# Kernel tuning notes

Hardware: AMD Instinct MI355X
Metric: run time of the kernel (lower is better)

The kernel has to match this reference:

```python
import jax, jax.numpy as jnp
import numpy as np

N_BLADES = 8

def _build_cayley():
    """Geometric-product table for Cl(3,0): C[i,j,k] s.t. (e_i * e_j) = sum_k C[i,j,k] e_k.
    Blade order: [1, e1, e2, e3, e12, e13, e23, e123] via bitmasks [0,1,2,4,3,5,6,7]."""
    blades = [0, 1, 2, 4, 3, 5, 6, 7]
    idx = {b: i for i, b in enumerate(blades)}
    C = np.zeros((8, 8, 8), dtype=np.float32)
    for i, a in enumerate(blades):
        for j, b in enumerate(blades):
            aa = a >> 1
            cnt = 0
            while aa:
                cnt += bin(aa & b).count('1')
                aa >>= 1
            sign = -1.0 if (cnt & 1) else 1.0
            C[i, j, idx[a ^ b]] += sign
    return jnp.asarray(C)

CAYLEY = _build_cayley()

def clifford_linear(x, w, b):
    # x: (..., 8), w: (8,), b: (8,) -> geometric product w * x + b
    return jnp.einsum('ijk,i,...j->...k', CAYLEY, w, x) + b

def setup_inputs() -> dict:
    key = jax.random.key(0)
    ks = jax.random.split(key, 9)
    B, S = 4, 4096
    inp = {'x': jax.random.normal(ks[0], (B, S, N_BLADES), dtype=jnp.float32)}
    names = ['wq', 'bq', 'wk', 'bk', 'wv', 'bv', 'wo', 'bo']
    for i, n in enumerate(names):
        scale = 1.0 / np.sqrt(N_BLADES) if n.startswith('w') else 0.02
        inp[n] = jax.random.normal(ks[i + 1], (N_BLADES,), dtype=jnp.float32) * scale
    return inp

def reference(x, wq, bq, wk, bk, wv, bv, wo, bo):
    # head_dim = max(1, 8 // 2) = 4 -> scale = sqrt(4) = 2
    scale = jnp.float32(2.0)
    Q = clifford_linear(x, wq, bq)  # (B,S,8)
    K = clifford_linear(x, wk, bk)
    V = clifford_linear(x, wv, bv)
    c0 = CAYLEY[..., 0]  # (8,8) scalar part of geometric product
    attn = jnp.einsum('ij,bsi,btj->bst', c0, Q, K) / scale  # (B,S,S)
    attn = jax.nn.softmax(attn, axis=-1)
    out = jnp.einsum('bst,btk->bsk', attn, V)  # (B,S,8)
    return clifford_linear(out, wo, bo)
```

## Files before the change

kernel.cpp:

```cpp
#include <hip/hip_runtime.h>
#include <math.h>

#define SEQ 4096
#define NBATCH 4
#define SGRP 64
#define TWAVES 16
#define TCHUNK (SEQ / TWAVES)
#define TT 32
#define VTILE 288

typedef _Float16 f16;
typedef __attribute__((ext_vector_type(8))) _Float16 f16x8;
typedef __attribute__((ext_vector_type(8))) __bf16 bf16x8;
typedef __attribute__((ext_vector_type(16))) float f32x16;
typedef __attribute__((ext_vector_type(4))) unsigned u32x4;
typedef __attribute__((ext_vector_type(2))) unsigned u32x2;

__device__ __forceinline__ float fexp2(float x) {
#if __has_builtin(__builtin_amdgcn_exp2f)
  return __builtin_amdgcn_exp2f(x);
#else
  return exp2f(x);
#endif
}

__device__ __forceinline__ u32x2 pswap(unsigned a, unsigned b) {
#if __has_builtin(__builtin_amdgcn_permlane32_swap)
  return __builtin_amdgcn_permlane32_swap(a, b, false, false);
#else
  asm volatile("v_permlane32_swap_b32 %0, %1" : "+v"(a), "+v"(b));
  u32x2 r; r[0] = a; r[1] = b; return r;
#endif
}

__device__ __forceinline__ unsigned exp2_pk_bf16(float a, float b) {
  unsigned e0 = __builtin_bit_cast(unsigned, fexp2(a));
  unsigned e1 = __builtin_bit_cast(unsigned, fexp2(b));
  return __builtin_amdgcn_perm(e1, e0, 0x07060302u);
}

__device__ __forceinline__ unsigned short f2bf(float f) {
  unsigned u = __builtin_bit_cast(unsigned, f);
  u += 0x7FFF + ((u >> 16) & 1);
  return (unsigned short)(u >> 16);
}

__device__ __forceinline__ float cl_sign(int amask, int bmask) {
  int cnt = 0, aa = amask >> 1;
  while (aa) { cnt += __popc(aa & bmask); aa >>= 1; }
  return (cnt & 1) ? -1.f : 1.f;
}

__global__ __launch_bounds__(128) void ck_qkv(const float* __restrict__ x,
                                              const float* __restrict__ wq,
                                              const float* __restrict__ bq,
                                              const float* __restrict__ wk,
                                              const float* __restrict__ bk,
                                              const float* __restrict__ wv,
                                              const float* __restrict__ bv,
                                              f16* __restrict__ Qp,
                                              f16* __restrict__ Kp,
                                              unsigned short* __restrict__ Vt) {
  __shared__ float Pl[288];
  const int blades[8] = {0, 1, 2, 4, 3, 5, 6, 7};
  int tid = threadIdx.x;

  if (tid < 64) {
    int j = tid >> 3, k = tid & 7;
    int bj = blades[j];
    float mq = 0.f, mk = 0.f, mv = 0.f;
    for (int i = 0; i < 8; ++i) {
      int ai = blades[i];
      if (blades[ai ^ bj] != k) continue;
      float sgn = cl_sign(ai, bj);
      mq += sgn * wq[i]; mk += sgn * wk[i]; mv += sgn * wv[i];
    }
    float c0 = cl_sign(blades[k], blades[k]);
    const float F = 0.72134752044448170368f;
    Pl[tid]       = mq * c0 * F;
    Pl[64 + tid]  = mk;
    Pl[128 + tid] = mv;
    if (j == 0) {
      Pl[256 + k] = bq[k] * c0 * F;
      Pl[264 + k] = bk[k];
      Pl[272 + k] = bv[k];
    }
  }
  __syncthreads();

  int row = blockIdx.x * 128 + tid;
  int b = row >> 12;
  int s = row & (SEQ - 1);
  const float4* x4 = (const float4*)(x + (size_t)row * 8);
  float4 xa = x4[0], xb = x4[1];
  float xr[8] = {xa.x, xa.y, xa.z, xa.w, xb.x, xb.y, xb.z, xb.w};
  float q[8], k[8], v[8];
#pragma unroll
  for (int c = 0; c < 8; ++c) { q[c] = Pl[256 + c]; k[c] = Pl[264 + c]; v[c] = Pl[272 + c]; }
#pragma unroll
  for (int j = 0; j < 8; ++j) {
    float xj = xr[j];
#pragma unroll
    for (int c = 0; c < 8; ++c) {
      q[c] = fmaf(xj, Pl[j * 8 + c], q[c]);
      k[c] = fmaf(xj, Pl[64 + j * 8 + c], k[c]);
      v[c] = fmaf(xj, Pl[128 + j * 8 + c], v[c]);
    }
  }
  f16x8 qa, qb, ka;
#pragma unroll
  for (int c = 0; c < 8; ++c) {
    f16 h = (f16)q[c];
    qa[c] = h;
    qb[c] = (f16)(q[c] - (float)h);
    ka[c] = (f16)k[c];
  }
  f16x8* qrow = (f16x8*)(Qp + (size_t)row * 16);
  qrow[0] = qa; qrow[1] = qb;
  *(f16x8*)(Kp + (size_t)row * 8) = ka;
  unsigned short* vt = Vt + ((size_t)b * (SEQ / 32) + (s >> 5)) * VTILE + (s & 31);
#pragma unroll
  for (int c = 0; c < 8; ++c) vt[c * 32] = f2bf(v[c]);
  vt[8 * 32] = 0x3F80;
}

__global__ __launch_bounds__(1024, 5) void ck_attn(const f16* __restrict__ Qp,
                                                   const f16* __restrict__ Kp,
                                                   const unsigned short* __restrict__ Vt,
                                                   const float* __restrict__ wo,
                                                   const float* __restrict__ bo,
                                                   float* __restrict__ out) {
  __shared__ float Lo[TWAVES][SGRP][9];
  __shared__ float MoL[72];

  const int tid = threadIdx.x;
  const int w = tid >> 6;
  const int lane = tid & 63;
  const int ls = lane & 31;
  const int hf = lane >> 5;
  const int rowbase = blockIdx.x * SGRP;
  const int b = rowbase >> 12;

  if (tid < 64) {
    const int blades[8] = {0, 1, 2, 4, 3, 5, 6, 7};
    int j = tid >> 3, k = tid & 7;
    int bj = blades[j];
    float mo = 0.f;
    for (int i = 0; i < 8; ++i) {
      int ai = blades[i];
      if (blades[ai ^ bj] != k) continue;
      mo += cl_sign(ai, bj) * wo[i];
    }
    MoL[tid] = mo;
    if (j == 0) MoL[64 + k] = bo[k];
  }

  f16x8 qf0 = *(const f16x8*)(Qp + (size_t)(rowbase + ls) * 16 + 8 * hf);
  f16x8 qf1 = *(const f16x8*)(Qp + (size_t)(rowbase + 32 + ls) * 16 + 8 * hf);

  f32x16 acc0 = {0.f, 0.f, 0.f, 0.f, 0.f, 0.f, 0.f, 0.f,
                 0.f, 0.f, 0.f, 0.f, 0.f, 0.f, 0.f, 0.f};
  f32x16 acc1 = acc0;
  const f32x16 zero = acc0;

  const f16* kbase = Kp + ((size_t)b * SEQ + w * TCHUNK + ls) * 8;
  const unsigned short* vbase =
      Vt + ((size_t)b * (SEQ / 32) + w * (TCHUNK / 32)) * VTILE +
      (ls <= 8 ? ls : 8) * 32 + 8 * hf;

  const int NIT = TCHUNK / TT;

#pragma unroll 1
  for (int it = 0; it < NIT; ++it) {
    const int t0 = it * TT;
    f16x8 kf = *(const f16x8*)(kbase + (size_t)t0 * 8);
    u32x4 v0 = *(const u32x4*)(vbase + (size_t)it * VTILE);
    u32x4 v1 = *(const u32x4*)(vbase + (size_t)it * VTILE + 16);

    f32x16 s0 = __builtin_amdgcn_mfma_f32_32x32x16_f16(kf, qf0, zero, 0, 0, 0);
    f32x16 s1 = __builtin_amdgcn_mfma_f32_32x32x16_f16(kf, qf1, zero, 0, 0, 0);

    {
      unsigned d0 = exp2_pk_bf16(s0[0], s0[1]);
      unsigned d1 = exp2_pk_bf16(s0[2], s0[3]);
      unsigned d2 = exp2_pk_bf16(s0[4], s0[5]);
      unsigned d3 = exp2_pk_bf16(s0[6], s0[7]);
      u32x2 r02 = pswap(d0, d2);
      u32x2 r13 = pswap(d1, d3);
      u32x4 pb0 = {r02[0], r13[0], r02[1], r13[1]};
      acc0 = __builtin_amdgcn_mfma_f32_32x32x16_bf16(
          __builtin_bit_cast(bf16x8, v0), __builtin_bit_cast(bf16x8, pb0), acc0, 0, 0, 0);
      unsigned d4 = exp2_pk_bf16(s0[8], s0[9]);
      unsigned d5 = exp2_pk_bf16(s0[10], s0[11]);
      unsigned d6 = exp2_pk_bf16(s0[12], s0[13]);
      unsigned d7 = exp2_pk_bf16(s0[14], s0[15]);
      u32x2 r46 = pswap(d4, d6);
      u32x2 r57 = pswap(d5, d7);
      u32x4 pb1 = {r46[0], r57[0], r46[1], r57[1]};
      acc0 = __builtin_amdgcn_mfma_f32_32x32x16_bf16(
          __builtin_bit_cast(bf16x8, v1), __builtin_bit_cast(bf16x8, pb1), acc0, 0, 0, 0);
    }
    {
      unsigned d0 = exp2_pk_bf16(s1[0], s1[1]);
      unsigned d1 = exp2_pk_bf16(s1[2], s1[3]);
      unsigned d2 = exp2_pk_bf16(s1[4], s1[5]);
      unsigned d3 = exp2_pk_bf16(s1[6], s1[7]);
      u32x2 r02 = pswap(d0, d2);
      u32x2 r13 = pswap(d1, d3);
      u32x4 pb0 = {r02[0], r13[0], r02[1], r13[1]};
      acc1 = __builtin_amdgcn_mfma_f32_32x32x16_bf16(
          __builtin_bit_cast(bf16x8, v0), __builtin_bit_cast(bf16x8, pb0), acc1, 0, 0, 0);
      unsigned d4 = exp2_pk_bf16(s1[8], s1[9]);
      unsigned d5 = exp2_pk_bf16(s1[10], s1[11]);
      unsigned d6 = exp2_pk_bf16(s1[12], s1[13]);
      unsigned d7 = exp2_pk_bf16(s1[14], s1[15]);
      u32x2 r46 = pswap(d4, d6);
      u32x2 r57 = pswap(d5, d7);
      u32x4 pb1 = {r46[0], r57[0], r46[1], r57[1]};
      acc1 = __builtin_amdgcn_mfma_f32_32x32x16_bf16(
          __builtin_bit_cast(bf16x8, v1), __builtin_bit_cast(bf16x8, pb1), acc1, 0, 0, 0);
    }
  }

  if (hf == 0) {
    Lo[w][ls][0] = acc0[0]; Lo[w][ls][1] = acc0[1];
    Lo[w][ls][2] = acc0[2]; Lo[w][ls][3] = acc0[3];
    Lo[w][ls][8] = acc0[4];
    Lo[w][32 + ls][0] = acc1[0]; Lo[w][32 + ls][1] = acc1[1];
    Lo[w][32 + ls][2] = acc1[2]; Lo[w][32 + ls][3] = acc1[3];
    Lo[w][32 + ls][8] = acc1[4];
  } else {
    Lo[w][ls][4] = acc0[0]; Lo[w][ls][5] = acc0[1];
    Lo[w][ls][6] = acc0[2]; Lo[w][ls][7] = acc0[3];
    Lo[w][32 + ls][4] = acc1[0]; Lo[w][32 + ls][5] = acc1[1];
    Lo[w][32 + ls][6] = acc1[2]; Lo[w][32 + ls][7] = acc1[3];
  }
  __syncthreads();

  if (tid < SGRP * 9) {
    int s = tid / 9, j = tid - s * 9;
    float sum = 0.f;
#pragma unroll
    for (int w2 = 0; w2 < TWAVES; ++w2) sum += Lo[w2][s][j];
    Lo[0][s][j] = sum;
  }
  __syncthreads();

  if (tid < SGRP * 8) {
    int s = tid >> 3, ko = tid & 7;
    float inv = 1.f / Lo[0][s][8];
    float a = MoL[64 + ko];
#pragma unroll
    for (int j = 0; j < 8; ++j) a = fmaf(Lo[0][s][j] * inv, MoL[j * 8 + ko], a);
    out[(size_t)(rowbase + s) * 8 + ko] = a;
  }
}

extern "C" void kernel_launch(void* const* d_in, const int* in_sizes, int n_in,
                              void* d_out, int out_size, void* d_ws, size_t ws_size,
                              hipStream_t stream) {
  const float* x  = (const float*)d_in[0];
  const float* wq = (const float*)d_in[1];
  const float* bq = (const float*)d_in[2];
  const float* wk = (const float*)d_in[3];
  const float* bk = (const float*)d_in[4];
  const float* wv = (const float*)d_in[5];
  const float* bv = (const float*)d_in[6];
  const float* wo = (const float*)d_in[7];
  const float* bo = (const float*)d_in[8];

  f16* Qp = (f16*)d_ws;
  f16* Kp = Qp + (size_t)NBATCH * SEQ * 16;
  unsigned short* Vt = (unsigned short*)(Kp + (size_t)NBATCH * SEQ * 8);
  float* outp = (float*)d_out;

  hipLaunchKernelGGL(ck_qkv, dim3(NBATCH * SEQ / 128), dim3(128), 0, stream,
                     x, wq, bq, wk, bk, wv, bv, Qp, Kp, Vt);
  hipLaunchKernelGGL(ck_attn, dim3(NBATCH * SEQ / SGRP), dim3(1024), 0, stream,
                     Qp, Kp, Vt, wo, bo, outp);
}
```

Measured before the change: 21.37 us.

## Split attention key range across blocks and combine partials in a separate kernel

The key dimension is now split across four blocks per query group, each with 8 waves instead of 16, so the grid grows from 256 to 1024 blocks of 512 threads. Each block writes unnormalised partial numerators and denominators to workspace, and a new combine kernel sums them, normalises, and applies the output Clifford projection. The aim is better CU occupancy and load balance than 256 large blocks give. In exchange it adds a third kernel launch and a global round-trip for the partial sums.

```diff
diff --git a/kernel.cpp b/kernel.cpp
--- a/kernel.cpp
+++ b/kernel.cpp
@@ -4,10 +4,12 @@
 #define SEQ 4096
 #define NBATCH 4
 #define SGRP 64
-#define TWAVES 16
-#define TCHUNK (SEQ / TWAVES)
+#define TWAVES 8
+#define TBLK 4
+#define TCH (SEQ / TBLK / TWAVES)
 #define TT 32
 #define VTILE 288
+#define NGRP (NBATCH * SEQ / SGRP)
 
 typedef _Float16 f16;
 typedef __attribute__((ext_vector_type(8))) _Float16 f16x8;
@@ -124,36 +126,22 @@
   vt[8 * 32] = 0x3F80;
 }
 
-__global__ __launch_bounds__(1024, 5) void ck_attn(const f16* __restrict__ Qp,
-                                                   const f16* __restrict__ Kp,
-                                                   const unsigned short* __restrict__ Vt,
-                                                   const float* __restrict__ wo,
-                                                   const float* __restrict__ bo,
-                                                   float* __restrict__ out) {
+__global__ __launch_bounds__(512, 4) void ck_attn(const f16* __restrict__ Qp,
+                                                  const f16* __restrict__ Kp,
+                                                  const unsigned short* __restrict__ Vt,
+                                                  float* __restrict__ Pt) {
   __shared__ float Lo[TWAVES][SGRP][9];
-  __shared__ float MoL[72];
 
   const int tid = threadIdx.x;
   const int w = tid >> 6;
   const int lane = tid & 63;
   const int ls = lane & 31;
   const int hf = lane >> 5;
-  const int rowbase = blockIdx.x * SGRP;
+  const int bg = blockIdx.x & (NGRP - 1);
+  const int tb = blockIdx.x >> 8;
+  const int rowbase = bg * SGRP;
   const int b = rowbase >> 12;
-
-  if (tid < 64) {
-    const int blades[8] = {0, 1, 2, 4, 3, 5, 6, 7};
-    int j = tid >> 3, k = tid & 7;
-    int bj = blades[j];
-    float mo = 0.f;
-    for (int i = 0; i < 8; ++i) {
-      int ai = blades[i];
-      if (blades[ai ^ bj] != k) continue;
-      mo += cl_sign(ai, bj) * wo[i];
-    }
-    MoL[tid] = mo;
-    if (j == 0) MoL[64 + k] = bo[k];
-  }
+  const int tbase = tb * (SEQ / TBLK);
 
   f16x8 qf0 = *(const f16x8*)(Qp + (size_t)(rowbase + ls) * 16 + 8 * hf);
   f16x8 qf1 = *(const f16x8*)(Qp + (size_t)(rowbase + 32 + ls) * 16 + 8 * hf);
@@ -163,12 +151,12 @@
   f32x16 acc1 = acc0;
   const f32x16 zero = acc0;
 
-  const f16* kbase = Kp + ((size_t)b * SEQ + w * TCHUNK + ls) * 8;
+  const f16* kbase = Kp + ((size_t)b * SEQ + tbase + w * TCH + ls) * 8;
   const unsigned short* vbase =
-      Vt + ((size_t)b * (SEQ / 32) + w * (TCHUNK / 32)) * VTILE +
+      Vt + ((size_t)b * (SEQ / 32) + (tbase >> 5) + w * (TCH / 32)) * VTILE +
       (ls <= 8 ? ls : 8) * 32 + 8 * hf;
 
-  const int NIT = TCHUNK / TT;
+  const int NIT = TCH / TT;
 
 #pragma unroll 1
   for (int it = 0; it < NIT; ++it) {
@@ -237,23 +225,56 @@
   }
   __syncthreads();
 
-  if (tid < SGRP * 9) {
-    int s = tid / 9, j = tid - s * 9;
+  float* pt = Pt + ((size_t)(bg * TBLK + tb) * SGRP) * 9;
+  for (int idx = tid; idx < SGRP * 9; idx += 512) {
+    int s = idx / 9, j = idx - s * 9;
     float sum = 0.f;
 #pragma unroll
     for (int w2 = 0; w2 < TWAVES; ++w2) sum += Lo[w2][s][j];
-    Lo[0][s][j] = sum;
+    pt[idx] = sum;
+  }
+}
+
+__global__ __launch_bounds__(256) void ck_comb(const float* __restrict__ Pt,
+                                               const float* __restrict__ wo,
+                                               const float* __restrict__ bo,
+                                               float* __restrict__ out) {
+  __shared__ float MoL[72];
+  const int tid = threadIdx.x;
+  if (tid < 64) {
+    const int blades[8] = {0, 1, 2, 4, 3, 5, 6, 7};
+    int j = tid >> 3, k = tid & 7;
+    int bj = blades[j];
+    float mo = 0.f;
+    for (int i = 0; i < 8; ++i) {
+      int ai = blades[i];
+      if (blades[ai ^ bj] != k) continue;
+      mo += cl_sign(ai, bj) * wo[i];
+    }
+    MoL[tid] = mo;
+    if (j == 0) MoL[64 + k] = bo[k];
   }
   __syncthreads();
 
-  if (tid < SGRP * 8) {
-    int s = tid >> 3, ko = tid & 7;
-    float inv = 1.f / Lo[0][s][8];
-    float a = MoL[64 + ko];
-#pragma unroll
-    for (int j = 0; j < 8; ++j) a = fmaf(Lo[0][s][j] * inv, MoL[j * 8 + ko], a);
-    out[(size_t)(rowbase + s) * 8 + ko] = a;
-  }
+  int g = blockIdx.x * 256 + tid;
+  int row = g >> 3, ko = g & 7;
+  int bg = row >> 6, s = row & (SGRP - 1);
+
+  const float* base = Pt + ((size_t)(bg * TBLK) * SGRP + s) * 9;
+  float sum[9];
+#pragma unroll
+  for (int j = 0; j < 9; ++j) sum[j] = 0.f;
+#pragma unroll
+  for (int tb = 0; tb < TBLK; ++tb) {
+    const float* p = base + (size_t)tb * SGRP * 9;
+#pragma unroll
+    for (int j = 0; j < 9; ++j) sum[j] += p[j];
+  }
+  float inv = 1.f / sum[8];
+  float a = MoL[64 + ko];
+#pragma unroll
+  for (int j = 0; j < 8; ++j) a = fmaf(sum[j] * inv, MoL[j * 8 + ko], a);
+  out[(size_t)row * 8 + ko] = a;
 }
 
 extern "C" void kernel_launch(void* const* d_in, const int* in_sizes, int n_in,
@@ -272,10 +293,13 @@
   f16* Qp = (f16*)d_ws;
   f16* Kp = Qp + (size_t)NBATCH * SEQ * 16;
   unsigned short* Vt = (unsigned short*)(Kp + (size_t)NBATCH * SEQ * 8);
+  float* Pt = (float*)(Vt + (size_t)NBATCH * (SEQ / 32) * VTILE);
   float* outp = (float*)d_out;
 
   hipLaunchKernelGGL(ck_qkv, dim3(NBATCH * SEQ / 128), dim3(128), 0, stream,
                      x, wq, bq, wk, bk, wv, bv, Qp, Kp, Vt);
-  hipLaunchKernelGGL(ck_attn, dim3(NBATCH * SEQ / SGRP), dim3(1024), 0, stream,
-                     Qp, Kp, Vt, wo, bo, outp);
-}
+  hipLaunchKernelGGL(ck_attn, dim3(NGRP * TBLK), dim3(512), 0, stream,
+                     Qp, Kp, Vt, Pt);
+  hipLaunchKernelGGL(ck_comb, dim3(NBATCH * SEQ * 8 / 256), dim3(256), 0, stream,
+                     Pt, wo, bo, outp);
+}
```

Result: slower. 24.86 us (+16.3%).
